# Kernel optimization log

Hardware: AMD Instinct MI355X
Metric: run time of the kernel (lower is better)

## Reference

```python
import jax, jax.numpy as jnp
import numpy as np

B, T, I, H, A, V, OOV = 256, 1, 256, 512, 400, 50000, 50


def _xavier(k, shape):
    fan_out, fan_in = shape[0], shape[-1]
    std = (2.0 / (fan_in + fan_out)) ** 0.5
    return jax.random.normal(k, shape, jnp.float32) * std


def setup_inputs() -> dict:
    key = jax.random.key(0)
    ks = jax.random.split(key, 24)
    return {
        "x": jax.random.normal(ks[0], (B, T, I), jnp.float32),
        "y": jax.random.randint(ks[1], (B, T), 0, V),  # teacher-forcing arg, unused in forward
        "encoder_outputs": jax.random.normal(ks[2], (B, A, A), jnp.float32),
        "encoder_cell": jax.random.normal(ks[3], (B, H), jnp.float32),  # encoder_in[1], unused
        "encoder_state": jax.random.normal(ks[4], (B, H), jnp.float32),
        "max_oov_nums": OOV,
        "ids": jax.random.randint(ks[5], (B, A), 0, V + OOV),
        # LSTM params (PyTorch layout: gates ordered i, f, g, o)
        "W_ih": jax.random.normal(ks[6], (4 * H, I), jnp.float32) * (1.0 / np.sqrt(H)),
        "W_hh": jax.random.normal(ks[7], (4 * H, H), jnp.float32) * (1.0 / np.sqrt(H)),
        "b_ih": jnp.zeros((4 * H,), jnp.float32),
        "b_hh": jnp.zeros((4 * H,), jnp.float32),
        # attention
        "Wh_w": _xavier(ks[8], (A, H)), "Wh_b": jnp.zeros((A,), jnp.float32),
        "Ws_w": _xavier(ks[9], (A, H)), "Ws_b": jnp.zeros((A,), jnp.float32),
        "v": jax.random.normal(ks[10], (A,), jnp.float32),
        # vocab head
        "fc1_w": _xavier(ks[11], (2 * H, H + A)), "fc1_b": jnp.zeros((2 * H,), jnp.float32),
        "fc2_w": _xavier(ks[12], (V, 2 * H)), "fc2_b": jnp.zeros((V,), jnp.float32),
        # p_gen gates (no bias)
        "pg1_w": _xavier(ks[13], (1, I)),
        "pg2_w": _xavier(ks[14], (1, A)),
        "pg3_w": _xavier(ks[15], (1, H)),
    }


def reference(x, y, encoder_outputs, encoder_cell, encoder_state, max_oov_nums, ids,
              W_ih, W_hh, b_ih, b_hh, Wh_w, Wh_b, Ws_w, Ws_b, v,
              fc1_w, fc1_b, fc2_w, fc2_b, pg1_w, pg2_w, pg3_w):
    x0 = x[:, 0, :]  # [B, I] single decode step
    # --- single LSTM step with zero initial (h, c) ---
    gates = x0 @ W_ih.T + b_ih + b_hh  # h0 = 0 so W_hh term vanishes
    i_g, f_g, g_g, o_g = jnp.split(gates, 4, axis=-1)
    c = jax.nn.sigmoid(i_g) * jnp.tanh(g_g)  # c0 = 0
    h = jax.nn.sigmoid(o_g) * jnp.tanh(c)    # decoder_state [B, H]
    # --- Bahdanau-style attention (first step: coverage is zeros, w_c has no bias) ---
    e = jnp.tanh(encoder_state @ Wh_w.T + Wh_b + h @ Ws_w.T + Ws_b)  # [B, A]
    attention = v * jax.nn.softmax(e, axis=-1)  # [B, A]
    # --- context vector: weighted sum over encoder outputs ---
    context = jnp.einsum('ba,bae->be', attention, encoder_outputs)  # [B, A]
    # --- vocab distribution ---
    dec_in = jnp.concatenate([context, h], axis=-1)  # [B, A+H]
    p_vocab = jax.nn.softmax((dec_in @ fc1_w.T + fc1_b) @ fc2_w.T + fc2_b, axis=-1)  # [B, V]
    # --- generation probability gate ---
    gen = jax.nn.sigmoid(context @ pg2_w[0] + x0 @ pg1_w[0] + h @ pg3_w[0])  # [B]
    p_vocab = gen[:, None] * p_vocab
    att_copy = (1.0 - gen)[:, None] * attention
    # --- extended vocab + copy scatter-add ---
    p = jnp.concatenate([p_vocab, jnp.zeros((p_vocab.shape[0], max_oov_nums), p_vocab.dtype)], axis=-1)
    rows = jnp.arange(p.shape[0])[:, None]
    p = p.at[rows, ids].add(att_copy)
    return p
```

## Files before the change

kernel.cpp:

```cpp
#include <hip/hip_runtime.h>
#include <hip/hip_bf16.h>
#include <math.h>

#define BB      256
#define I_DIM   256
#define H_DIM   512
#define A_DIM   400
#define V_DIM   50000
#define OOV     50
#define VP      50050
#define FC1_IN  912
#define FC1_OUT 1024
#define FC2_K   1024

typedef unsigned short u16;
typedef unsigned int   u32;
typedef __attribute__((ext_vector_type(8))) short  short8;
typedef __attribute__((ext_vector_type(4))) float  float4_;

__device__ __forceinline__ u16 f2bf(float f) {
    u32 u = __builtin_bit_cast(u32, f);
    u32 r = (u + 0x7FFFu + ((u >> 16) & 1u)) >> 16;
    return (u16)r;
}

__global__ __launch_bounds__(256)
void sgemm32(const float* __restrict__ Am, const float* __restrict__ Wm,
             float* __restrict__ Cm, const float* __restrict__ bias0,
             const float* __restrict__ bias1, int M, int N, int K,
             int accumulate, int act)
{
    __shared__ float As[16][33];
    __shared__ float Bs[16][33];
    int t  = threadIdx.x;
    int tx = t & 15, ty = t >> 4;
    int m0 = blockIdx.y * 32, n0 = blockIdx.x * 32;
    int lm = t >> 3;
    int lk = (t & 7) * 2;
    const float* aptr = Am + (size_t)(m0 + lm) * K + lk;
    const float* wptr = Wm + (size_t)(n0 + lm) * K + lk;
    bool wvalid = (n0 + lm) < N;
    float c00 = 0.f, c01 = 0.f, c10 = 0.f, c11 = 0.f;

    for (int k0 = 0; k0 < K; k0 += 16) {
        float a0 = aptr[0], a1 = aptr[1];
        float w0 = wvalid ? wptr[0] : 0.f;
        float w1 = wvalid ? wptr[1] : 0.f;
        __syncthreads();
        As[lk][lm] = a0;  As[lk + 1][lm] = a1;
        Bs[lk][lm] = w0;  Bs[lk + 1][lm] = w1;
        __syncthreads();
#pragma unroll
        for (int k = 0; k < 16; ++k) {
            float av0 = As[k][ty], av1 = As[k][ty + 16];
            float bv0 = Bs[k][tx], bv1 = Bs[k][tx + 16];
            c00 += av0 * bv0;  c01 += av0 * bv1;
            c10 += av1 * bv0;  c11 += av1 * bv1;
        }
        aptr += 16; wptr += 16;
    }

    int r0 = m0 + ty, r1 = m0 + ty + 16;
    int cc0 = n0 + tx, cc1 = n0 + tx + 16;
    float accv[2][2] = {{c00, c01}, {c10, c11}};
    int rows[2] = {r0, r1};
    int cols[2] = {cc0, cc1};
#pragma unroll
    for (int i = 0; i < 2; ++i)
#pragma unroll
        for (int j = 0; j < 2; ++j) {
            int c = cols[j];
            if (c < N) {
                size_t idx = (size_t)rows[i] * N + c;
                float v = accv[i][j];
                if (accumulate) v += Cm[idx];
                if (bias0) v += bias0[c];
                if (bias1) v += bias1[c];
                if (act == 1) v = tanhf(v);
                Cm[idx] = v;
            }
        }
}

__global__ __launch_bounds__(256)
void lstm_h_kernel(const float* __restrict__ G, float* __restrict__ hbuf,
                   float* __restrict__ dec_in)
{
    int idx = blockIdx.x * 256 + threadIdx.x;
    int b = idx >> 9, j = idx & 511;
    const float* g = G + (size_t)b * 2048;
    float ig = g[j], gg = g[1024 + j], og = g[1536 + j];
    float si = 1.f / (1.f + expf(-ig));
    float so = 1.f / (1.f + expf(-og));
    float c  = si * tanhf(gg);
    float h  = so * tanhf(c);
    hbuf[idx] = h;
    dec_in[(size_t)b * FC1_IN + A_DIM + j] = h;
}

__global__ __launch_bounds__(256)
void att_kernel(const float* __restrict__ e, const float* __restrict__ vvec,
                float* __restrict__ att)
{
    __shared__ float s_ex[A_DIM];
    __shared__ float red[256];
    int b = blockIdx.x, t = threadIdx.x;
    const float* er = e + (size_t)b * A_DIM;
    float local = 0.f;
    for (int a = t; a < A_DIM; a += 256) {
        float ex = expf(er[a]);
        s_ex[a] = ex; local += ex;
    }
    red[t] = local; __syncthreads();
    for (int s = 128; s > 0; s >>= 1) {
        if (t < s) red[t] += red[t + s];
        __syncthreads();
    }
    float inv = 1.f / red[0];
    for (int a = t; a < A_DIM; a += 256)
        att[(size_t)b * A_DIM + a] = vvec[a] * s_ex[a] * inv;
}

__global__ __launch_bounds__(512)
void ctx_gen_kernel(const float* __restrict__ att, const float* __restrict__ enc,
                    const float* __restrict__ x, const float* __restrict__ h,
                    const float* __restrict__ pg1, const float* __restrict__ pg2,
                    const float* __restrict__ pg3,
                    float* __restrict__ dec_in, float* __restrict__ gen)
{
    __shared__ float s_att[A_DIM];
    __shared__ float red[512];
    int b = blockIdx.x, t = threadIdx.x;
    for (int a = t; a < A_DIM; a += 512) s_att[a] = att[(size_t)b * A_DIM + a];
    __syncthreads();
    float acc = 0.f;
    if (t < A_DIM) {
        const float* ep = enc + (size_t)b * (A_DIM * A_DIM) + t;
#pragma unroll 4
        for (int a = 0; a < A_DIM; ++a) acc += s_att[a] * ep[(size_t)a * A_DIM];
        dec_in[(size_t)b * FC1_IN + t] = acc;
    }
    float local = 0.f;
    if (t < A_DIM) local += acc * pg2[t];
    if (t < I_DIM) local += x[(size_t)b * I_DIM + t] * pg1[t];
    local += h[(size_t)b * H_DIM + t] * pg3[t];
    red[t] = local; __syncthreads();
    for (int s = 256; s > 0; s >>= 1) {
        if (t < s) red[t] += red[t + s];
        __syncthreads();
    }
    if (t == 0) gen[b] = 1.f / (1.f + expf(-red[0]));
}

__global__ __launch_bounds__(256)
void cvt_kernel(const float* __restrict__ hid, u16* __restrict__ hb)
{
    int idx = blockIdx.x * 256 + threadIdx.x;
    hb[idx] = f2bf(hid[idx]);
}

__global__ __launch_bounds__(256)
void fc2_kernel(const u16* __restrict__ hb, const float* __restrict__ W,
                const float* __restrict__ bias, float* __restrict__ out,
                float* __restrict__ sums)
{
    __shared__ __align__(16) u16 Ws[64][72];
    int t = threadIdx.x;
    int wv = t >> 6, lane = t & 63;
    int lm = lane & 15, lk = lane >> 4;
    int n0 = blockIdx.x * 64;
    int row_base = wv * 64;

    float4_ acc[4][4];
#pragma unroll
    for (int mi = 0; mi < 4; ++mi)
#pragma unroll
        for (int ni = 0; ni < 4; ++ni)
            acc[mi][ni] = (float4_){0.f, 0.f, 0.f, 0.f};

    int sn  = t >> 2;
    int skq = (t & 3) * 16;
    bool svalid = (n0 + sn) < V_DIM;
    const float* wsrc = W + (size_t)(n0 + sn) * FC2_K + skq;

    for (int kt = 0; kt < FC2_K / 64; ++kt) {
        float4_ wreg[4];
        if (svalid) {
            const float4_* p = (const float4_*)(wsrc + kt * 64);
            wreg[0] = p[0]; wreg[1] = p[1]; wreg[2] = p[2]; wreg[3] = p[3];
        } else {
#pragma unroll
            for (int i = 0; i < 4; ++i) wreg[i] = (float4_){0.f, 0.f, 0.f, 0.f};
        }
        __syncthreads();
        short8 wlo, whi;
#pragma unroll
        for (int i = 0; i < 4; ++i) {
            wlo[i]     = (short)f2bf(wreg[0][i]);
            wlo[4 + i] = (short)f2bf(wreg[1][i]);
            whi[i]     = (short)f2bf(wreg[2][i]);
            whi[4 + i] = (short)f2bf(wreg[3][i]);
        }
        *(short8*)&Ws[sn][skq]     = wlo;
        *(short8*)&Ws[sn][skq + 8] = whi;
        __syncthreads();

#pragma unroll
        for (int ks = 0; ks < 2; ++ks) {
            short8 af[4], bfr[4];
#pragma unroll
            for (int mi = 0; mi < 4; ++mi)
                af[mi] = *(const short8*)(hb + (size_t)(row_base + mi * 16 + lm) * FC2_K
                                          + kt * 64 + ks * 32 + lk * 8);
#pragma unroll
            for (int ni = 0; ni < 4; ++ni)
                bfr[ni] = *(const short8*)&Ws[ni * 16 + lm][ks * 32 + lk * 8];
#pragma unroll
            for (int mi = 0; mi < 4; ++mi)
#pragma unroll
                for (int ni = 0; ni < 4; ++ni)
                    acc[mi][ni] = __builtin_amdgcn_mfma_f32_16x16x32_bf16(
                        af[mi], bfr[ni], acc[mi][ni], 0, 0, 0);
        }
    }

#pragma unroll
    for (int mi = 0; mi < 4; ++mi) {
        int r_base = row_base + mi * 16 + lk * 4;
        float s[4] = {0.f, 0.f, 0.f, 0.f};
#pragma unroll
        for (int ni = 0; ni < 4; ++ni) {
            int col = n0 + ni * 16 + lm;
            if (col < V_DIM) {
                float bcol = bias[col];
                float4_ a = acc[mi][ni];
#pragma unroll
                for (int r = 0; r < 4; ++r) {
                    float ev = expf(a[r] + bcol);
                    out[(size_t)(r_base + r) * VP + col] = ev;
                    s[r] += ev;
                }
            }
        }
#pragma unroll
        for (int off = 1; off < 16; off <<= 1) {
#pragma unroll
            for (int r = 0; r < 4; ++r) s[r] += __shfl_xor(s[r], off);
        }
        if (lm == 0) {
#pragma unroll
            for (int r = 0; r < 4; ++r) atomicAdd(&sums[r_base + r], s[r]);
        }
    }
}

__global__ __launch_bounds__(256)
void rescale_kernel(float* __restrict__ out, const float* __restrict__ gen,
                    const float* __restrict__ sums)
{
    int idx = (blockIdx.x * 256 + threadIdx.x) * 2;
    int b = idx / VP;
    int c = idx - b * VP;
    float2 v = *(float2*)(out + idx);
    float scale = gen[b] / sums[b];
    v.x = (c     < V_DIM) ? v.x * scale : 0.f;
    v.y = (c + 1 < V_DIM) ? v.y * scale : 0.f;
    *(float2*)(out + idx) = v;
}

__global__ __launch_bounds__(256)
void scatter_kernel(const int* __restrict__ ids, const float* __restrict__ att,
                    const float* __restrict__ gen, float* __restrict__ out)
{
    int idx = blockIdx.x * 256 + threadIdx.x;
    int b = idx / A_DIM;
    float val = (1.f - gen[b]) * att[idx];
    atomicAdd(out + (size_t)b * VP + ids[idx], val);
}

extern "C" void kernel_launch(void* const* d_in, const int* in_sizes, int n_in,
                              void* d_out, int out_size, void* d_ws, size_t ws_size,
                              hipStream_t stream)
{
    const float* x         = (const float*)d_in[0];
    const float* enc       = (const float*)d_in[2];
    const float* enc_state = (const float*)d_in[4];
    const int*   ids       = (const int*)  d_in[6];
    const float* W_ih      = (const float*)d_in[7];
    const float* b_ih      = (const float*)d_in[9];
    const float* b_hh      = (const float*)d_in[10];
    const float* Wh_w      = (const float*)d_in[11];
    const float* Wh_b      = (const float*)d_in[12];
    const float* Ws_w      = (const float*)d_in[13];
    const float* Ws_b      = (const float*)d_in[14];
    const float* vvec      = (const float*)d_in[15];
    const float* fc1_w     = (const float*)d_in[16];
    const float* fc1_b     = (const float*)d_in[17];
    const float* fc2_w     = (const float*)d_in[18];
    const float* fc2_b     = (const float*)d_in[19];
    const float* pg1       = (const float*)d_in[20];
    const float* pg2       = (const float*)d_in[21];
    const float* pg3       = (const float*)d_in[22];
    float* out = (float*)d_out;

    float* ws    = (float*)d_ws;
    float* gates = ws;
    float* hbuf  = gates + 256 * 2048;
    float* ebuf  = hbuf  + 256 * 512;
    float* attb  = ebuf  + 256 * 400;
    float* dec   = attb  + 256 * 400;
    float* hid   = dec   + 256 * 912;
    float* genb  = hid   + 256 * 1024;
    float* sums  = genb  + 256;
    u16*   hbf   = (u16*)(sums + 256);

    sgemm32<<<dim3(64, 8), 256, 0, stream>>>(x, W_ih, gates, b_ih, b_hh,
                                             BB, 2048, I_DIM, 0, 0);
    lstm_h_kernel<<<512, 256, 0, stream>>>(gates, hbuf, dec);
    sgemm32<<<dim3(13, 8), 256, 0, stream>>>(enc_state, Wh_w, ebuf, Wh_b, nullptr,
                                             BB, A_DIM, H_DIM, 0, 0);
    sgemm32<<<dim3(13, 8), 256, 0, stream>>>(hbuf, Ws_w, ebuf, Ws_b, nullptr,
                                             BB, A_DIM, H_DIM, 1, 1);
    att_kernel<<<BB, 256, 0, stream>>>(ebuf, vvec, attb);
    ctx_gen_kernel<<<BB, 512, 0, stream>>>(attb, enc, x, hbuf, pg1, pg2, pg3,
                                           dec, genb);
    sgemm32<<<dim3(32, 8), 256, 0, stream>>>(dec, fc1_w, hid, fc1_b, nullptr,
                                             BB, FC1_OUT, FC1_IN, 0, 0);
    cvt_kernel<<<1024, 256, 0, stream>>>(hid, hbf);
    hipMemsetAsync(sums, 0, BB * sizeof(float), stream);
    fc2_kernel<<<782, 256, 0, stream>>>(hbf, fc2_w, fc2_b, out, sums);
    rescale_kernel<<<(BB * VP) / 512, 256, 0, stream>>>(out, genb, sums);
    scatter_kernel<<<(BB * A_DIM) / 256, 256, 0, stream>>>(ids, attb, genb, out);
}
```

Before: 768.2 us.

## Restructure fc2 GEMM to drop LDS staging, split rows across grid, packed bf16 convert

The fc2 kernel no longer stages converted weight tiles in shared memory with barriers. Each wave now loads its own fp32 weight rows directly, converts them with a packed bf16 conversion instruction when available, and feeds the MFMAs. The grid gains a second dimension that splits the batch rows, so each wave owns a 64x32 output tile, which doubles the block count. This removes barriers and LDS traffic at the cost of more redundant global weight reads per block pair. The context reduction also gets four independent accumulators, and the sums memset is moved to the start of the launch sequence.

```diff
diff --git a/kernel.cpp b/kernel.cpp
--- a/kernel.cpp
+++ b/kernel.cpp
@@ -17,12 +17,25 @@
 typedef unsigned int   u32;
 typedef __attribute__((ext_vector_type(8))) short  short8;
 typedef __attribute__((ext_vector_type(4))) float  float4_;
+typedef __attribute__((ext_vector_type(4))) u32    uint4_;
 
 __device__ __forceinline__ u16 f2bf(float f) {
     u32 u = __builtin_bit_cast(u32, f);
     u32 r = (u + 0x7FFFu + ((u >> 16) & 1u)) >> 16;
     return (u16)r;
 }
+
+#if __has_builtin(__builtin_amdgcn_cvt_pk_bf16_f32)
+typedef __attribute__((ext_vector_type(2))) __bf16 bf16x2_t;
+__device__ __forceinline__ u32 pk2bf(float lo, float hi) {
+    bf16x2_t r = __builtin_amdgcn_cvt_pk_bf16_f32(lo, hi);
+    return __builtin_bit_cast(u32, r);
+}
+#else
+__device__ __forceinline__ u32 pk2bf(float lo, float hi) {
+    return (u32)f2bf(lo) | ((u32)f2bf(hi) << 16);
+}
+#endif
 
 __global__ __launch_bounds__(256)
 void sgemm32(const float* __restrict__ Am, const float* __restrict__ Wm,
@@ -136,8 +149,15 @@
     float acc = 0.f;
     if (t < A_DIM) {
         const float* ep = enc + (size_t)b * (A_DIM * A_DIM) + t;
-#pragma unroll 4
-        for (int a = 0; a < A_DIM; ++a) acc += s_att[a] * ep[(size_t)a * A_DIM];
+        float a0 = 0.f, a1 = 0.f, a2 = 0.f, a3 = 0.f;
+#pragma unroll 2
+        for (int a = 0; a < A_DIM; a += 4) {
+            a0 += s_att[a]     * ep[(size_t)a * A_DIM];
+            a1 += s_att[a + 1] * ep[(size_t)(a + 1) * A_DIM];
+            a2 += s_att[a + 2] * ep[(size_t)(a + 2) * A_DIM];
+            a3 += s_att[a + 3] * ep[(size_t)(a + 3) * A_DIM];
+        }
+        acc = (a0 + a1) + (a2 + a3);
         dec_in[(size_t)b * FC1_IN + t] = acc;
     }
     float local = 0.f;
@@ -164,72 +184,60 @@
                 const float* __restrict__ bias, float* __restrict__ out,
                 float* __restrict__ sums)
 {
-    __shared__ __align__(16) u16 Ws[64][72];
     int t = threadIdx.x;
     int wv = t >> 6, lane = t & 63;
     int lm = lane & 15, lk = lane >> 4;
-    int n0 = blockIdx.x * 64;
-    int row_base = wv * 64;
-
-    float4_ acc[4][4];
+    int rh = wv & 1, ch = wv >> 1;
+    int n0   = blockIdx.x * 64 + ch * 32;
+    int row0 = blockIdx.y * 128 + rh * 64;
+
+    float4_ acc[4][2];
 #pragma unroll
     for (int mi = 0; mi < 4; ++mi)
 #pragma unroll
-        for (int ni = 0; ni < 4; ++ni)
+        for (int ni = 0; ni < 2; ++ni)
             acc[mi][ni] = (float4_){0.f, 0.f, 0.f, 0.f};
 
-    int sn  = t >> 2;
-    int skq = (t & 3) * 16;
-    bool svalid = (n0 + sn) < V_DIM;
-    const float* wsrc = W + (size_t)(n0 + sn) * FC2_K + skq;
-
-    for (int kt = 0; kt < FC2_K / 64; ++kt) {
-        float4_ wreg[4];
-        if (svalid) {
-            const float4_* p = (const float4_*)(wsrc + kt * 64);
-            wreg[0] = p[0]; wreg[1] = p[1]; wreg[2] = p[2]; wreg[3] = p[3];
-        } else {
-#pragma unroll
-            for (int i = 0; i < 4; ++i) wreg[i] = (float4_){0.f, 0.f, 0.f, 0.f};
-        }
-        __syncthreads();
-        short8 wlo, whi;
-#pragma unroll
-        for (int i = 0; i < 4; ++i) {
-            wlo[i]     = (short)f2bf(wreg[0][i]);
-            wlo[4 + i] = (short)f2bf(wreg[1][i]);
-            whi[i]     = (short)f2bf(wreg[2][i]);
-            whi[4 + i] = (short)f2bf(wreg[3][i]);
-        }
-        *(short8*)&Ws[sn][skq]     = wlo;
-        *(short8*)&Ws[sn][skq + 8] = whi;
-        __syncthreads();
-
-#pragma unroll
-        for (int ks = 0; ks < 2; ++ks) {
-            short8 af[4], bfr[4];
-#pragma unroll
-            for (int mi = 0; mi < 4; ++mi)
-                af[mi] = *(const short8*)(hb + (size_t)(row_base + mi * 16 + lm) * FC2_K
-                                          + kt * 64 + ks * 32 + lk * 8);
-#pragma unroll
-            for (int ni = 0; ni < 4; ++ni)
-                bfr[ni] = *(const short8*)&Ws[ni * 16 + lm][ks * 32 + lk * 8];
-#pragma unroll
-            for (int mi = 0; mi < 4; ++mi)
-#pragma unroll
-                for (int ni = 0; ni < 4; ++ni)
-                    acc[mi][ni] = __builtin_amdgcn_mfma_f32_16x16x32_bf16(
-                        af[mi], bfr[ni], acc[mi][ni], 0, 0, 0);
-        }
+    const u16* aptr = hb + (size_t)(row0 + lm) * FC2_K + lk * 8;
+    int wr0 = n0 + lm;        if (wr0 > V_DIM - 1) wr0 = V_DIM - 1;
+    int wr1 = n0 + 16 + lm;   if (wr1 > V_DIM - 1) wr1 = V_DIM - 1;
+    const float* wp0 = W + (size_t)wr0 * FC2_K + lk * 8;
+    const float* wp1 = W + (size_t)wr1 * FC2_K + lk * 8;
+
+    for (int k0 = 0; k0 < FC2_K; k0 += 32) {
+        short8 af[4];
+#pragma unroll
+        for (int mi = 0; mi < 4; ++mi)
+            af[mi] = *(const short8*)(aptr + (size_t)mi * 16 * FC2_K + k0);
+        float4_ w00 = *(const float4_*)(wp0 + k0);
+        float4_ w01 = *(const float4_*)(wp0 + k0 + 4);
+        float4_ w10 = *(const float4_*)(wp1 + k0);
+        float4_ w11 = *(const float4_*)(wp1 + k0 + 4);
+
+        uint4_ p0, p1;
+        p0[0] = pk2bf(w00[0], w00[1]);  p0[1] = pk2bf(w00[2], w00[3]);
+        p0[2] = pk2bf(w01[0], w01[1]);  p0[3] = pk2bf(w01[2], w01[3]);
+        p1[0] = pk2bf(w10[0], w10[1]);  p1[1] = pk2bf(w10[2], w10[3]);
+        p1[2] = pk2bf(w11[0], w11[1]);  p1[3] = pk2bf(w11[2], w11[3]);
+        short8 bf0 = __builtin_bit_cast(short8, p0);
+        short8 bf1 = __builtin_bit_cast(short8, p1);
+
+#pragma unroll
+        for (int mi = 0; mi < 4; ++mi)
+            acc[mi][0] = __builtin_amdgcn_mfma_f32_16x16x32_bf16(af[mi], bf0,
+                                                                 acc[mi][0], 0, 0, 0);
+#pragma unroll
+        for (int mi = 0; mi < 4; ++mi)
+            acc[mi][1] = __builtin_amdgcn_mfma_f32_16x16x32_bf16(af[mi], bf1,
+                                                                 acc[mi][1], 0, 0, 0);
     }
 
 #pragma unroll
     for (int mi = 0; mi < 4; ++mi) {
-        int r_base = row_base + mi * 16 + lk * 4;
+        int r_base = row0 + mi * 16 + lk * 4;
         float s[4] = {0.f, 0.f, 0.f, 0.f};
 #pragma unroll
-        for (int ni = 0; ni < 4; ++ni) {
+        for (int ni = 0; ni < 2; ++ni) {
             int col = n0 + ni * 16 + lm;
             if (col < V_DIM) {
                 float bcol = bias[col];
@@ -314,6 +322,8 @@
     float* sums  = genb  + 256;
     u16*   hbf   = (u16*)(sums + 256);
 
+    hipMemsetAsync(sums, 0, BB * sizeof(float), stream);
+
     sgemm32<<<dim3(64, 8), 256, 0, stream>>>(x, W_ih, gates, b_ih, b_hh,
                                              BB, 2048, I_DIM, 0, 0);
     lstm_h_kernel<<<512, 256, 0, stream>>>(gates, hbuf, dec);
@@ -327,8 +337,7 @@
     sgemm32<<<dim3(32, 8), 256, 0, stream>>>(dec, fc1_w, hid, fc1_b, nullptr,
                                              BB, FC1_OUT, FC1_IN, 0, 0);
     cvt_kernel<<<1024, 256, 0, stream>>>(hid, hbf);
-    hipMemsetAsync(sums, 0, BB * sizeof(float), stream);
-    fc2_kernel<<<782, 256, 0, stream>>>(hbf, fc2_w, fc2_b, out, sums);
+    fc2_kernel<<<dim3(782, 2), 256, 0, stream>>>(hbf, fc2_w, fc2_b, out, sums);
     rescale_kernel<<<(BB * VP) / 512, 256, 0, stream>>>(out, genb, sums);
     scatter_kernel<<<(BB * A_DIM) / 256, 256, 0, stream>>>(ids, attb, genb, out);
 }
```

Result: slower. 924.6 us (+20.4%).
